# Kernel optimization log

Hardware: AMD Instinct MI355X
Metric: run time of the kernel (lower is better)

Reference implementation:

```python
import jax, jax.numpy as jnp
import numpy as np

N_NODES = 100000
N_EDGES = 1600000
N_FEAT = 128
HIDDEN = 128
N_GRAPHS = 1024


def setup_inputs() -> dict:
    key = jax.random.key(0)
    ks = jax.random.split(key, 9)
    x = jax.random.normal(ks[0], (N_NODES, N_FEAT), dtype=jnp.float32)
    edge_index = jax.random.randint(ks[1], (2, N_EDGES), 0, N_NODES, dtype=jnp.int64)
    batch = jnp.sort(jax.random.randint(ks[2], (N_NODES,), 0, N_GRAPHS, dtype=jnp.int64))
    W1 = jax.random.normal(ks[3], (N_FEAT, HIDDEN), dtype=jnp.float32) * (1.0 / np.sqrt(N_FEAT))
    b1 = jax.random.normal(ks[4], (HIDDEN,), dtype=jnp.float32) * 0.01
    W2 = jax.random.normal(ks[5], (HIDDEN, HIDDEN), dtype=jnp.float32) * (1.0 / np.sqrt(HIDDEN))
    b2 = jax.random.normal(ks[6], (HIDDEN,), dtype=jnp.float32) * 0.01
    Wl = jax.random.normal(ks[7], (HIDDEN, 2), dtype=jnp.float32) * (1.0 / np.sqrt(HIDDEN))
    bl = jax.random.normal(ks[8], (2,), dtype=jnp.float32) * 0.01
    return {"x": x, "edge_index": edge_index, "batch": batch,
            "W1": W1, "b1": b1, "W2": W2, "b2": b2, "Wl": Wl, "bl": bl}


def _gcn_norm(edge_index, num_nodes):
    # PyG GCNConv: add self-loops, then sym-normalize with in-degree (target col).
    loop = jnp.arange(num_nodes, dtype=edge_index.dtype)
    src = jnp.concatenate([edge_index[0], loop])  # [E+N]
    dst = jnp.concatenate([edge_index[1], loop])  # [E+N]
    deg = jax.ops.segment_sum(jnp.ones_like(dst, dtype=jnp.float32), dst,
                              num_segments=num_nodes)
    dinv = jnp.where(deg > 0, jax.lax.rsqrt(deg), 0.0)
    norm = dinv[src] * dinv[dst]  # [E+N]
    return src, dst, norm


def _gcn_conv(h, W, b, src, dst, norm, num_nodes):
    h = h @ W                                   # [N, out]
    msg = h[src] * norm[:, None]                # gather + scale, [E+N, out]
    agg = jax.ops.segment_sum(msg, dst, num_segments=num_nodes)  # scatter-add
    return agg + b


def reference(x, edge_index, batch, W1, b1, W2, b2, Wl, bl):
    n = x.shape[0]
    src, dst, norm = _gcn_norm(edge_index, n)
    h = jax.nn.relu(_gcn_conv(x, W1, b1, src, dst, norm, n))
    h = jax.nn.relu(_gcn_conv(h, W2, b2, src, dst, norm, n))
    # global_mean_pool over graph ids
    sums = jax.ops.segment_sum(h, batch, num_segments=N_GRAPHS)        # [G, H]
    counts = jax.ops.segment_sum(jnp.ones((n,), jnp.float32), batch,
                                 num_segments=N_GRAPHS)
    pooled = sums / jnp.maximum(counts, 1.0)[:, None]
    # F.dropout with training=False default in inference -> identity
    return pooled @ Wl + bl  # [G, 2]
```

## Files before the change

### kernel.cpp

```cpp
#include <hip/hip_runtime.h>
#include <hip/hip_bf16.h>

#define N_NODES 100000
#define N_EDGES 1600000
#define FEAT 128
#define N_GRAPHS 1024
#define NBUCK 391
#define CHUNK 4096

typedef short short8 __attribute__((ext_vector_type(8)));
typedef float float4v __attribute__((ext_vector_type(4)));

static __device__ inline unsigned short f2bf(float f) {
    __hip_bfloat16 b = __float2bfloat16(f);
    unsigned short r;
    __builtin_memcpy(&r, &b, 2);
    return r;
}
static __device__ inline float bf_lo(unsigned int v) { return __uint_as_float(v << 16); }
static __device__ inline float bf_hi(unsigned int v) { return __uint_as_float(v & 0xFFFF0000u); }
static __device__ inline float bf_s(unsigned short s) { return __uint_as_float(((unsigned)s) << 16); }

__global__ __launch_bounds__(256) void k_prep(const float* __restrict__ W1,
                                              const float* __restrict__ W2,
                                              unsigned short* __restrict__ wp1,
                                              unsigned short* __restrict__ wp2,
                                              int* __restrict__ bcount,
                                              unsigned int* __restrict__ udummy) {
    int bid = blockIdx.x;
    const float* W = (bid < 64) ? W1 : W2;
    unsigned short* wp = (bid < 64) ? wp1 : wp2;
    int t = (bid & 63) * 256 + threadIdx.x;
    int k = t >> 7, n = t & 127;
    float w = W[k * 128 + n];
    unsigned ub = __float_as_uint(w);
    unsigned short hi = (unsigned short)(ub >> 16);
    float hif = __uint_as_float(ub & 0xFFFF0000u);
    unsigned short lo = f2bf(w - hif);
    int sidx = n * 128 + ((k & 7) | (8 * (((k >> 3) ^ n) & 15)));
    wp[sidx] = hi;
    wp[16384 + sidx] = lo;
    if (bid == 0) {
        for (int i = threadIdx.x; i < NBUCK; i += 256) bcount[i] = 0;
        if (threadIdx.x < 64) udummy[threadIdx.x] = 0;
    }
}

__global__ __launch_bounds__(256) void k_hist(const int* __restrict__ dst,
                                              int* __restrict__ bcount) {
    __shared__ int h[NBUCK];
    for (int i = threadIdx.x; i < NBUCK; i += 256) h[i] = 0;
    __syncthreads();
    for (int e = blockIdx.x * 256 + threadIdx.x; e < N_EDGES; e += gridDim.x * 256)
        atomicAdd(&h[dst[e] >> 8], 1);
    __syncthreads();
    for (int i = threadIdx.x; i < NBUCK; i += 256) {
        int c = h[i];
        if (c) atomicAdd(&bcount[i], c);
    }
}

__global__ __launch_bounds__(512) void k_scan391(const int* __restrict__ in,
                                                 int* __restrict__ base,
                                                 int* __restrict__ cur,
                                                 int* __restrict__ tail) {
    int t = threadIdx.x;
    int v = (t < NBUCK) ? in[t] : 0;
    int lane = t & 63, wid = t >> 6;
    int s = v;
#pragma unroll
    for (int d = 1; d < 64; d <<= 1) { int n = __shfl_up(s, d); if (lane >= d) s += n; }
    __shared__ int ws[8];
    if (lane == 63) ws[wid] = s;
    __syncthreads();
    if (t < 8) {
        int x = ws[t];
#pragma unroll
        for (int d = 1; d < 8; d <<= 1) { int n = __shfl_up(x, d); if ((int)t >= d) x += n; }
        ws[t] = x;
    }
    __syncthreads();
    int excl = s - v + (wid ? ws[wid - 1] : 0);
    if (t < NBUCK) {
        base[t] = excl;
        if (cur) cur[t] = excl;
    }
    if (t == 0 && tail) tail[0] = N_EDGES;
}

__global__ __launch_bounds__(256) void k_bucket(const int* __restrict__ src,
                                                const int* __restrict__ dst,
                                                int* __restrict__ bcur,
                                                unsigned int* __restrict__ pairs) {
    __shared__ int cnt[NBUCK];
    __shared__ int basebuf[NBUCK];
    int t = threadIdx.x;
    int e0 = blockIdx.x * CHUNK;
    for (int i = t; i < NBUCK; i += 256) cnt[i] = 0;
    __syncthreads();
    unsigned pk[16]; int bk[16];
#pragma unroll
    for (int j = 0; j < 16; ++j) {
        int e = e0 + j * 256 + t;
        if (e < N_EDGES) {
            int s = src[e], d = dst[e];
            bk[j] = d >> 8;
            pk[j] = ((unsigned)s << 8) | (unsigned)(d & 255);
            atomicAdd(&cnt[bk[j]], 1);
        } else bk[j] = -1;
    }
    __syncthreads();
    for (int i = t; i < NBUCK; i += 256) {
        int c = cnt[i];
        basebuf[i] = c ? atomicAdd(&bcur[i], c) : 0;
        cnt[i] = 0;
    }
    __syncthreads();
#pragma unroll
    for (int j = 0; j < 16; ++j) {
        if (bk[j] >= 0) {
            int p = basebuf[bk[j]] + atomicAdd(&cnt[bk[j]], 1);
            pairs[p] = pk[j];
        }
    }
}

__global__ __launch_bounds__(256) void k_bdeg(const unsigned int* __restrict__ pairs,
                                              const int* __restrict__ bbase,
                                              const int* __restrict__ bcount,
                                              int* __restrict__ deg,
                                              float* __restrict__ dinv,
                                              int* __restrict__ wsum) {
    __shared__ int d[256];
    __shared__ int wr[4];
    int b = blockIdx.x, t = threadIdx.x;
    d[t] = 0;
    __syncthreads();
    int s0 = bbase[b], n = bcount[b];
    for (int i = t; i < n; i += 256) atomicAdd(&d[pairs[s0 + i] & 255u], 1);
    __syncthreads();
    int node = b * 256 + t;
    int v = d[t];
    if (node < N_NODES) {
        deg[node] = v;
        dinv[node] = rsqrtf((float)(v + 1));
    }
#pragma unroll
    for (int dd = 32; dd > 0; dd >>= 1) v += __shfl_down(v, dd);
    if ((t & 63) == 0) wr[t >> 6] = v;
    __syncthreads();
    if (t == 0) wsum[b] = wr[0] + wr[1] + wr[2] + wr[3];
}

__global__ __launch_bounds__(256) void k_bfill(const unsigned int* __restrict__ pairs,
                                               const int* __restrict__ bbase,
                                               const int* __restrict__ bcount,
                                               const int* __restrict__ deg,
                                               const int* __restrict__ wbase,
                                               int* __restrict__ offs,
                                               int* __restrict__ csr) {
    __shared__ int lcur[256];
    __shared__ int ws[4];
    int b = blockIdx.x, t = threadIdx.x;
    int node = b * 256 + t;
    int dv = (node < N_NODES) ? deg[node] : 0;
    int lane = t & 63, wid = t >> 6;
    int s = dv;
#pragma unroll
    for (int d = 1; d < 64; d <<= 1) { int n = __shfl_up(s, d); if (lane >= d) s += n; }
    if (lane == 63) ws[wid] = s;
    __syncthreads();
    if (t < 4) {
        int x = ws[t];
#pragma unroll
        for (int d = 1; d < 4; d <<= 1) { int n = __shfl_up(x, d); if ((int)t >= d) x += n; }
        ws[t] = x;
    }
    __syncthreads();
    int excl = s - dv + (wid ? ws[wid - 1] : 0) + wbase[b];
    if (node < N_NODES) offs[node] = excl;
    lcur[t] = excl;
    __syncthreads();
    int s0 = bbase[b], n = bcount[b];
    for (int i = t; i < n; i += 256) {
        unsigned pr = pairs[s0 + i];
        int p = atomicAdd(&lcur[pr & 255u], 1);
        csr[p] = (int)(pr >> 8);
    }
}

__global__ __launch_bounds__(256) void k_gemm_mfma(const float* __restrict__ inp,
                                                   const unsigned short* __restrict__ wp,
                                                   const float* __restrict__ dinv,
                                                   unsigned short* __restrict__ u) {
    __shared__ unsigned short sW[32768];
    {
        float4* d4 = (float4*)sW;
        const float4* s4 = (const float4*)wp;
#pragma unroll
        for (int i = 0; i < 16; ++i) d4[threadIdx.x + 256 * i] = s4[threadIdx.x + 256 * i];
    }
    __syncthreads();
    const int t = threadIdx.x;
    const int wv = t >> 6, L = t & 63;
    const int m = L & 15, q = L >> 4;
    const int r0 = blockIdx.x * 64 + wv * 16;
    int arow = r0 + m;
    if (arow >= N_NODES) arow = N_NODES - 1;
    const float4* ap = (const float4*)(inp + (size_t)arow * 128);
    float4v acc[8];
#pragma unroll
    for (int c = 0; c < 8; ++c) acc[c] = (float4v){0.f, 0.f, 0.f, 0.f};

#pragma unroll
    for (int k0 = 0; k0 < 128; k0 += 32) {
        float4 f0 = ap[(k0 >> 2) + 2 * q];
        float4 f1 = ap[(k0 >> 2) + 2 * q + 1];
        float fa[8] = {f0.x, f0.y, f0.z, f0.w, f1.x, f1.y, f1.z, f1.w};
        short8 ah, al;
#pragma unroll
        for (int j = 0; j < 8; ++j) {
            unsigned ub = __float_as_uint(fa[j]);
            ah[j] = (short)(ub >> 16);
            float hif = __uint_as_float(ub & 0xFFFF0000u);
            al[j] = (short)f2bf(fa[j] - hif);
        }
        const int b = (k0 >> 3) + q;
#pragma unroll
        for (int c = 0; c < 8; ++c) {
            int ng = c * 16 + m;
            int elem = ng * 128 + 8 * ((b ^ ng) & 15);
            short8 bh = *(const short8*)&sW[elem];
            short8 bl = *(const short8*)&sW[16384 + elem];
            acc[c] = __builtin_amdgcn_mfma_f32_16x16x32_bf16(ah, bh, acc[c], 0, 0, 0);
            acc[c] = __builtin_amdgcn_mfma_f32_16x16x32_bf16(al, bh, acc[c], 0, 0, 0);
            acc[c] = __builtin_amdgcn_mfma_f32_16x16x32_bf16(ah, bl, acc[c], 0, 0, 0);
        }
    }
#pragma unroll
    for (int r = 0; r < 4; ++r) {
        int row = r0 + 4 * q + r;
        if (row < N_NODES) {
            float dv = dinv[row];
            unsigned short* up = u + (size_t)row * 128 + m;
#pragma unroll
            for (int c = 0; c < 8; ++c) up[c * 16] = f2bf(dv * acc[c][r]);
        }
    }
}

__global__ __launch_bounds__(256) void k_gemm_mfma_bf(const unsigned short* __restrict__ hh,
                                                      const unsigned short* __restrict__ hl,
                                                      const unsigned short* __restrict__ wp,
                                                      const float* __restrict__ dinv,
                                                      unsigned short* __restrict__ u) {
    __shared__ unsigned short sW[32768];
    {
        float4* d4 = (float4*)sW;
        const float4* s4 = (const float4*)wp;
#pragma unroll
        for (int i = 0; i < 16; ++i) d4[threadIdx.x + 256 * i] = s4[threadIdx.x + 256 * i];
    }
    __syncthreads();
    const int t = threadIdx.x;
    const int wv = t >> 6, L = t & 63;
    const int m = L & 15, q = L >> 4;
    const int r0 = blockIdx.x * 64 + wv * 16;
    int arow = r0 + m;
    if (arow >= N_NODES) arow = N_NODES - 1;
    const unsigned short* hhp = hh + (size_t)arow * 128 + 8 * q;
    const unsigned short* hlp = hl + (size_t)arow * 128 + 8 * q;
    float4v acc[8];
#pragma unroll
    for (int c = 0; c < 8; ++c) acc[c] = (float4v){0.f, 0.f, 0.f, 0.f};

#pragma unroll
    for (int k0 = 0; k0 < 128; k0 += 32) {
        short8 ah = *(const short8*)(hhp + k0);
        short8 al = *(const short8*)(hlp + k0);
        const int b = (k0 >> 3) + q;
#pragma unroll
        for (int c = 0; c < 8; ++c) {
            int ng = c * 16 + m;
            int elem = ng * 128 + 8 * ((b ^ ng) & 15);
            short8 bh = *(const short8*)&sW[elem];
            short8 bl = *(const short8*)&sW[16384 + elem];
            acc[c] = __builtin_amdgcn_mfma_f32_16x16x32_bf16(ah, bh, acc[c], 0, 0, 0);
            acc[c] = __builtin_amdgcn_mfma_f32_16x16x32_bf16(al, bh, acc[c], 0, 0, 0);
            acc[c] = __builtin_amdgcn_mfma_f32_16x16x32_bf16(ah, bl, acc[c], 0, 0, 0);
        }
    }
#pragma unroll
    for (int r = 0; r < 4; ++r) {
        int row = r0 + 4 * q + r;
        if (row < N_NODES) {
            float dv = dinv[row];
            unsigned short* up = u + (size_t)row * 128 + m;
#pragma unroll
            for (int c = 0; c < 8; ++c) up[c * 16] = f2bf(dv * acc[c][r]);
        }
    }
}

__global__ __launch_bounds__(256) void k_agg(const unsigned int* __restrict__ u,
                                             const int* __restrict__ offs,
                                             const int* __restrict__ csr,
                                             const float* __restrict__ dinv,
                                             const float* __restrict__ bias,
                                             unsigned int* __restrict__ hhp,
                                             unsigned int* __restrict__ hlp) {
    int wid = threadIdx.x >> 6;
    int lane = threadIdx.x & 63;
    int node = __builtin_amdgcn_readfirstlane(blockIdx.x * 4 + wid);
    if (node >= N_NODES) return;
    int p = __builtin_amdgcn_readfirstlane(offs[node]);
    int e = __builtin_amdgcn_readfirstlane(offs[node + 1]);
    unsigned int self = u[(size_t)node * 64 + lane];
    float ax0 = bf_lo(self), ay0 = bf_hi(self);
    float ax1 = 0.f, ay1 = 0.f, ax2 = 0.f, ay2 = 0.f, ax3 = 0.f, ay3 = 0.f;
    float ax4 = 0.f, ay4 = 0.f, ax5 = 0.f, ay5 = 0.f, ax6 = 0.f, ay6 = 0.f;
    float ax7 = 0.f, ay7 = 0.f;
    for (; p < e; p += 8) {
        int c0 = csr[p + 0], c1 = csr[p + 1], c2 = csr[p + 2], c3 = csr[p + 3];
        int c4 = csr[p + 4], c5 = csr[p + 5], c6 = csr[p + 6], c7 = csr[p + 7];
        int i0 = c0;
        int i1 = (p + 1 < e) ? c1 : N_NODES;
        int i2 = (p + 2 < e) ? c2 : N_NODES;
        int i3 = (p + 3 < e) ? c3 : N_NODES;
        int i4 = (p + 4 < e) ? c4 : N_NODES;
        int i5 = (p + 5 < e) ? c5 : N_NODES;
        int i6 = (p + 6 < e) ? c6 : N_NODES;
        int i7 = (p + 7 < e) ? c7 : N_NODES;
        unsigned v0 = (u + (size_t)i0 * 64)[lane];
        unsigned v1 = (u + (size_t)i1 * 64)[lane];
        unsigned v2 = (u + (size_t)i2 * 64)[lane];
        unsigned v3 = (u + (size_t)i3 * 64)[lane];
        unsigned v4 = (u + (size_t)i4 * 64)[lane];
        unsigned v5 = (u + (size_t)i5 * 64)[lane];
        unsigned v6 = (u + (size_t)i6 * 64)[lane];
        unsigned v7 = (u + (size_t)i7 * 64)[lane];
        ax0 += bf_lo(v0); ay0 += bf_hi(v0);
        ax1 += bf_lo(v1); ay1 += bf_hi(v1);
        ax2 += bf_lo(v2); ay2 += bf_hi(v2);
        ax3 += bf_lo(v3); ay3 += bf_hi(v3);
        ax4 += bf_lo(v4); ay4 += bf_hi(v4);
        ax5 += bf_lo(v5); ay5 += bf_hi(v5);
        ax6 += bf_lo(v6); ay6 += bf_hi(v6);
        ax7 += bf_lo(v7); ay7 += bf_hi(v7);
    }
    float d = dinv[node];
    float2 b = ((const float2*)bias)[lane];
    float sx = ((ax0 + ax1) + (ax2 + ax3)) + ((ax4 + ax5) + (ax6 + ax7));
    float sy = ((ay0 + ay1) + (ay2 + ay3)) + ((ay4 + ay5) + (ay6 + ay7));
    float r0 = fmaxf(d * sx + b.x, 0.f);
    float r1 = fmaxf(d * sy + b.y, 0.f);
    if (hlp) {
        unsigned u0 = __float_as_uint(r0), u1 = __float_as_uint(r1);
        unsigned short h0 = (unsigned short)(u0 >> 16), h1 = (unsigned short)(u1 >> 16);
        float rf0 = __uint_as_float(u0 & 0xFFFF0000u), rf1 = __uint_as_float(u1 & 0xFFFF0000u);
        unsigned short l0 = f2bf(r0 - rf0), l1 = f2bf(r1 - rf1);
        hhp[(size_t)node * 64 + lane] = (unsigned)h0 | ((unsigned)h1 << 16);
        hlp[(size_t)node * 64 + lane] = (unsigned)l0 | ((unsigned)l1 << 16);
    } else {
        hhp[(size_t)node * 64 + lane] = (unsigned)f2bf(r0) | ((unsigned)f2bf(r1) << 16);
    }
}

__global__ __launch_bounds__(128) void k_pool(const unsigned short* __restrict__ hh,
                                              const int* __restrict__ batch,
                                              const float* __restrict__ Wl,
                                              const float* __restrict__ bl,
                                              float* __restrict__ out) {
    int g = blockIdx.x;
    int c = threadIdx.x;
    __shared__ int sb[2];
    if (c < 2) {
        int tgt = g + c;
        int lo = 0, hi = N_NODES;
        while (lo < hi) { int m = (lo + hi) >> 1; if (batch[m] < tgt) lo = m + 1; else hi = m; }
        sb[c] = lo;
    }
    __syncthreads();
    int s0 = sb[0], s1 = sb[1];
    float sum = 0.f;
    for (int i = s0; i < s1; ++i) sum += bf_s(hh[(size_t)i * 128 + c]);
    float cnt = (float)(s1 - s0);
    float pooled = sum / fmaxf(cnt, 1.0f);
    __shared__ float red[128];
    float w0 = Wl[c * 2 + 0], w1 = Wl[c * 2 + 1];
    red[c] = pooled * w0;
    __syncthreads();
    for (int st = 64; st > 0; st >>= 1) { if (c < st) red[c] += red[c + st]; __syncthreads(); }
    if (c == 0) out[g * 2 + 0] = red[0] + bl[0];
    __syncthreads();
    red[c] = pooled * w1;
    __syncthreads();
    for (int st = 64; st > 0; st >>= 1) { if (c < st) red[c] += red[c + st]; __syncthreads(); }
    if (c == 0) out[g * 2 + 1] = red[0] + bl[1];
}

extern "C" void kernel_launch(void* const* d_in, const int* in_sizes, int n_in,
                              void* d_out, int out_size, void* d_ws, size_t ws_size,
                              hipStream_t stream) {
    const float* x  = (const float*)d_in[0];
    const int* ei   = (const int*)d_in[1];
    const int* batch = (const int*)d_in[2];
    const float* W1 = (const float*)d_in[3];
    const float* b1 = (const float*)d_in[4];
    const float* W2 = (const float*)d_in[5];
    const float* b2 = (const float*)d_in[6];
    const float* Wl = (const float*)d_in[7];
    const float* bl = (const float*)d_in[8];
    float* out = (float*)d_out;
    const int* src = ei;
    const int* dst = ei + N_EDGES;

    char* ws = (char*)d_ws;
    size_t o = 0;
    auto alloc = [&](size_t bytes) -> void* {
        o = (o + 255) & ~(size_t)255;
        void* p = ws + o;
        o += bytes;
        return p;
    };
    int* bcount = (int*)alloc((size_t)NBUCK * 4);
    int* bbase  = (int*)alloc((size_t)NBUCK * 4);
    int* bcur   = (int*)alloc((size_t)NBUCK * 4);
    int* wsum   = (int*)alloc((size_t)NBUCK * 4);
    int* wbase  = (int*)alloc((size_t)NBUCK * 4);
    int* deg    = (int*)alloc((size_t)N_NODES * 4);
    float* dinv = (float*)alloc((size_t)N_NODES * 4);
    int* offs   = (int*)alloc((size_t)(N_NODES + 1) * 4);
    unsigned short* wp1 = (unsigned short*)alloc(65536);
    unsigned short* wp2 = (unsigned short*)alloc(65536);
    unsigned int* pairs = (unsigned int*)alloc((size_t)N_EDGES * 4);
    int* csr    = (int*)alloc((size_t)(N_EDGES + 8) * 4);
    unsigned short* u = (unsigned short*)alloc((size_t)(N_NODES + 1) * 128 * 2);
    unsigned short* hh = (unsigned short*)alloc((size_t)N_NODES * 128 * 2);
    unsigned short* hl = (unsigned short*)alloc((size_t)N_NODES * 128 * 2);

    k_prep<<<128, 256, 0, stream>>>(W1, W2, wp1, wp2, bcount,
                                    (unsigned int*)(u + (size_t)N_NODES * 128));
    k_hist<<<256, 256, 0, stream>>>(dst, bcount);
    k_scan391<<<1, 512, 0, stream>>>(bcount, bbase, bcur, nullptr);
    k_bucket<<<(N_EDGES + CHUNK - 1) / CHUNK, 256, 0, stream>>>(src, dst, bcur, pairs);
    k_bdeg<<<NBUCK, 256, 0, stream>>>(pairs, bbase, bcount, deg, dinv, wsum);
    k_scan391<<<1, 512, 0, stream>>>(wsum, wbase, nullptr, &offs[N_NODES]);
    k_bfill<<<NBUCK, 256, 0, stream>>>(pairs, bbase, bcount, deg, wbase, offs, csr);

    const int gemmGrid = (N_NODES + 63) / 64;
    k_gemm_mfma<<<gemmGrid, 256, 0, stream>>>(x, wp1, dinv, u);
    k_agg<<<(N_NODES + 3) / 4, 256, 0, stream>>>((const unsigned int*)u, offs, csr, dinv, b1,
                                                 (unsigned int*)hh, (unsigned int*)hl);
    k_gemm_mfma_bf<<<gemmGrid, 256, 0, stream>>>(hh, hl, wp2, dinv, u);
    k_agg<<<(N_NODES + 3) / 4, 256, 0, stream>>>((const unsigned int*)u, offs, csr, dinv, b2,
                                                 (unsigned int*)hh, nullptr);

    k_pool<<<N_GRAPHS, 128, 0, stream>>>(hh, batch, Wl, bl, out);
}
```

Measured before the change: 362.6 us.

## Overlap first GEMM with CSR build and fold degree pass into fill

The first layer's GEMM no longer needs dinv, because the source-side normalization moves into the aggregation kernel. That lets the GEMM tiles run as extra blocks inside the bucket and fill kernels, so they overlap with CSR construction. The separate degree kernel and second scan are merged into the fill kernel, which computes local degrees and uses the bucket base as the offset. The weight-prep and histogram kernels are also fused into one launch. In exchange, the aggregation now does an extra dinv gather per neighbor, and the mixed blocks carry a large shared-memory footprint that may reduce occupancy for the bucket blocks.

```diff
diff --git a/kernel.cpp b/kernel.cpp
--- a/kernel.cpp
+++ b/kernel.cpp
@@ -7,6 +7,9 @@
 #define N_GRAPHS 1024
 #define NBUCK 391
 #define CHUNK 4096
+#define NTILES 1563
+#define G1A 781
+#define G1B 782
 
 typedef short short8 __attribute__((ext_vector_type(8)));
 typedef float float4v __attribute__((ext_vector_type(4)));
@@ -21,42 +24,44 @@
 static __device__ inline float bf_hi(unsigned int v) { return __uint_as_float(v & 0xFFFF0000u); }
 static __device__ inline float bf_s(unsigned short s) { return __uint_as_float(((unsigned)s) << 16); }
 
-__global__ __launch_bounds__(256) void k_prep(const float* __restrict__ W1,
-                                              const float* __restrict__ W2,
-                                              unsigned short* __restrict__ wp1,
-                                              unsigned short* __restrict__ wp2,
-                                              int* __restrict__ bcount,
-                                              unsigned int* __restrict__ udummy) {
+__global__ __launch_bounds__(256) void k_prep_hist(const float* __restrict__ W1,
+                                                   const float* __restrict__ W2,
+                                                   unsigned short* __restrict__ wp1,
+                                                   unsigned short* __restrict__ wp2,
+                                                   const int* __restrict__ dst,
+                                                   int* __restrict__ bcount,
+                                                   unsigned int* __restrict__ udummy,
+                                                   float* __restrict__ dinv) {
     int bid = blockIdx.x;
-    const float* W = (bid < 64) ? W1 : W2;
-    unsigned short* wp = (bid < 64) ? wp1 : wp2;
-    int t = (bid & 63) * 256 + threadIdx.x;
-    int k = t >> 7, n = t & 127;
-    float w = W[k * 128 + n];
-    unsigned ub = __float_as_uint(w);
-    unsigned short hi = (unsigned short)(ub >> 16);
-    float hif = __uint_as_float(ub & 0xFFFF0000u);
-    unsigned short lo = f2bf(w - hif);
-    int sidx = n * 128 + ((k & 7) | (8 * (((k >> 3) ^ n) & 15)));
-    wp[sidx] = hi;
-    wp[16384 + sidx] = lo;
-    if (bid == 0) {
-        for (int i = threadIdx.x; i < NBUCK; i += 256) bcount[i] = 0;
-        if (threadIdx.x < 64) udummy[threadIdx.x] = 0;
-    }
-}
-
-__global__ __launch_bounds__(256) void k_hist(const int* __restrict__ dst,
-                                              int* __restrict__ bcount) {
-    __shared__ int h[NBUCK];
-    for (int i = threadIdx.x; i < NBUCK; i += 256) h[i] = 0;
-    __syncthreads();
-    for (int e = blockIdx.x * 256 + threadIdx.x; e < N_EDGES; e += gridDim.x * 256)
-        atomicAdd(&h[dst[e] >> 8], 1);
-    __syncthreads();
-    for (int i = threadIdx.x; i < NBUCK; i += 256) {
-        int c = h[i];
-        if (c) atomicAdd(&bcount[i], c);
+    if (bid < 128) {
+        const float* W = (bid < 64) ? W1 : W2;
+        unsigned short* wp = (bid < 64) ? wp1 : wp2;
+        int t = (bid & 63) * 256 + threadIdx.x;
+        int k = t >> 7, n = t & 127;
+        float w = W[k * 128 + n];
+        unsigned ub = __float_as_uint(w);
+        unsigned short hi = (unsigned short)(ub >> 16);
+        float hif = __uint_as_float(ub & 0xFFFF0000u);
+        unsigned short lo = f2bf(w - hif);
+        int sidx = n * 128 + ((k & 7) | (8 * (((k >> 3) ^ n) & 15)));
+        wp[sidx] = hi;
+        wp[16384 + sidx] = lo;
+        if (bid == 0) {
+            if (threadIdx.x < 64) udummy[threadIdx.x] = 0;
+            if (threadIdx.x == 64) dinv[N_NODES] = 0.f;
+        }
+    } else {
+        __shared__ int h[NBUCK];
+        for (int i = threadIdx.x; i < NBUCK; i += 256) h[i] = 0;
+        __syncthreads();
+        int hb = bid - 128;
+        for (int e = hb * 256 + threadIdx.x; e < N_EDGES; e += 256 * 256)
+            atomicAdd(&h[dst[e] >> 8], 1);
+        __syncthreads();
+        for (int i = threadIdx.x; i < NBUCK; i += 256) {
+            int c = h[i];
+            if (c) atomicAdd(&bcount[i], c);
+        }
     }
 }
 
@@ -83,15 +88,79 @@
     int excl = s - v + (wid ? ws[wid - 1] : 0);
     if (t < NBUCK) {
         base[t] = excl;
-        if (cur) cur[t] = excl;
-    }
-    if (t == 0 && tail) tail[0] = N_EDGES;
-}
-
-__global__ __launch_bounds__(256) void k_bucket(const int* __restrict__ src,
-                                                const int* __restrict__ dst,
-                                                int* __restrict__ bcur,
-                                                unsigned int* __restrict__ pairs) {
+        cur[t] = excl;
+    }
+    if (t == 0) tail[0] = N_EDGES;
+}
+
+__device__ __forceinline__ void gemm_f32_body(int tile, const float* __restrict__ inp,
+                                              const unsigned short* __restrict__ wp,
+                                              unsigned short* __restrict__ u) {
+    __shared__ unsigned short sW[32768];
+    {
+        float4* d4 = (float4*)sW;
+        const float4* s4 = (const float4*)wp;
+#pragma unroll
+        for (int i = 0; i < 16; ++i) d4[threadIdx.x + 256 * i] = s4[threadIdx.x + 256 * i];
+    }
+    __syncthreads();
+    const int t = threadIdx.x;
+    const int wv = t >> 6, L = t & 63;
+    const int m = L & 15, q = L >> 4;
+    const int r0 = tile * 64 + wv * 16;
+    int arow = r0 + m;
+    if (arow >= N_NODES) arow = N_NODES - 1;
+    const float4* ap = (const float4*)(inp + (size_t)arow * 128);
+    float4v acc[8];
+#pragma unroll
+    for (int c = 0; c < 8; ++c) acc[c] = (float4v){0.f, 0.f, 0.f, 0.f};
+#pragma unroll
+    for (int k0 = 0; k0 < 128; k0 += 32) {
+        float4 f0 = ap[(k0 >> 2) + 2 * q];
+        float4 f1 = ap[(k0 >> 2) + 2 * q + 1];
+        float fa[8] = {f0.x, f0.y, f0.z, f0.w, f1.x, f1.y, f1.z, f1.w};
+        short8 ah, al;
+#pragma unroll
+        for (int j = 0; j < 8; ++j) {
+            unsigned ub = __float_as_uint(fa[j]);
+            ah[j] = (short)(ub >> 16);
+            float hif = __uint_as_float(ub & 0xFFFF0000u);
+            al[j] = (short)f2bf(fa[j] - hif);
+        }
+        const int b = (k0 >> 3) + q;
+#pragma unroll
+        for (int c = 0; c < 8; ++c) {
+            int ng = c * 16 + m;
+            int elem = ng * 128 + 8 * ((b ^ ng) & 15);
+            short8 bh = *(const short8*)&sW[elem];
+            short8 bl = *(const short8*)&sW[16384 + elem];
+            acc[c] = __builtin_amdgcn_mfma_f32_16x16x32_bf16(ah, bh, acc[c], 0, 0, 0);
+            acc[c] = __builtin_amdgcn_mfma_f32_16x16x32_bf16(al, bh, acc[c], 0, 0, 0);
+            acc[c] = __builtin_amdgcn_mfma_f32_16x16x32_bf16(ah, bl, acc[c], 0, 0, 0);
+        }
+    }
+#pragma unroll
+    for (int r = 0; r < 4; ++r) {
+        int row = r0 + 4 * q + r;
+        if (row < N_NODES) {
+            unsigned short* up = u + (size_t)row * 128 + m;
+#pragma unroll
+            for (int c = 0; c < 8; ++c) up[c * 16] = f2bf(acc[c][r]);
+        }
+    }
+}
+
+__global__ __launch_bounds__(256) void k_bucket_g1(const int* __restrict__ src,
+                                                   const int* __restrict__ dst,
+                                                   int* __restrict__ bcur,
+                                                   unsigned int* __restrict__ pairs,
+                                                   const float* __restrict__ x,
+                                                   const unsigned short* __restrict__ wp1,
+                                                   unsigned short* __restrict__ u) {
+    if (blockIdx.x >= NBUCK) {
+        gemm_f32_body(blockIdx.x - NBUCK, x, wp1, u);
+        return;
+    }
     __shared__ int cnt[NBUCK];
     __shared__ int basebuf[NBUCK];
     int t = threadIdx.x;
@@ -125,63 +194,48 @@
     }
 }
 
-__global__ __launch_bounds__(256) void k_bdeg(const unsigned int* __restrict__ pairs,
-                                              const int* __restrict__ bbase,
-                                              const int* __restrict__ bcount,
-                                              int* __restrict__ deg,
-                                              float* __restrict__ dinv,
-                                              int* __restrict__ wsum) {
-    __shared__ int d[256];
-    __shared__ int wr[4];
-    int b = blockIdx.x, t = threadIdx.x;
-    d[t] = 0;
-    __syncthreads();
-    int s0 = bbase[b], n = bcount[b];
-    for (int i = t; i < n; i += 256) atomicAdd(&d[pairs[s0 + i] & 255u], 1);
-    __syncthreads();
-    int node = b * 256 + t;
-    int v = d[t];
-    if (node < N_NODES) {
-        deg[node] = v;
-        dinv[node] = rsqrtf((float)(v + 1));
-    }
-#pragma unroll
-    for (int dd = 32; dd > 0; dd >>= 1) v += __shfl_down(v, dd);
-    if ((t & 63) == 0) wr[t >> 6] = v;
-    __syncthreads();
-    if (t == 0) wsum[b] = wr[0] + wr[1] + wr[2] + wr[3];
-}
-
-__global__ __launch_bounds__(256) void k_bfill(const unsigned int* __restrict__ pairs,
-                                               const int* __restrict__ bbase,
-                                               const int* __restrict__ bcount,
-                                               const int* __restrict__ deg,
-                                               const int* __restrict__ wbase,
-                                               int* __restrict__ offs,
-                                               int* __restrict__ csr) {
+__global__ __launch_bounds__(256) void k_bfill_g1(const unsigned int* __restrict__ pairs,
+                                                  const int* __restrict__ bbase,
+                                                  const int* __restrict__ bcount,
+                                                  float* __restrict__ dinv,
+                                                  int* __restrict__ offs,
+                                                  int* __restrict__ csr,
+                                                  const float* __restrict__ x,
+                                                  const unsigned short* __restrict__ wp1,
+                                                  unsigned short* __restrict__ u) {
+    if (blockIdx.x >= NBUCK) {
+        gemm_f32_body(blockIdx.x - NBUCK + G1A, x, wp1, u);
+        return;
+    }
+    __shared__ int degl[256];
     __shared__ int lcur[256];
     __shared__ int ws[4];
     int b = blockIdx.x, t = threadIdx.x;
+    degl[t] = 0;
+    __syncthreads();
+    int s0 = bbase[b], n = bcount[b];
+    for (int i = t; i < n; i += 256) atomicAdd(&degl[pairs[s0 + i] & 255u], 1);
+    __syncthreads();
     int node = b * 256 + t;
-    int dv = (node < N_NODES) ? deg[node] : 0;
+    int dv = degl[t];
+    if (node < N_NODES) dinv[node] = rsqrtf((float)(dv + 1));
     int lane = t & 63, wid = t >> 6;
     int s = dv;
 #pragma unroll
-    for (int d = 1; d < 64; d <<= 1) { int n = __shfl_up(s, d); if (lane >= d) s += n; }
+    for (int d = 1; d < 64; d <<= 1) { int nn = __shfl_up(s, d); if (lane >= d) s += nn; }
     if (lane == 63) ws[wid] = s;
     __syncthreads();
     if (t < 4) {
-        int x = ws[t];
-#pragma unroll
-        for (int d = 1; d < 4; d <<= 1) { int n = __shfl_up(x, d); if ((int)t >= d) x += n; }
-        ws[t] = x;
-    }
-    __syncthreads();
-    int excl = s - dv + (wid ? ws[wid - 1] : 0) + wbase[b];
+        int xx = ws[t];
+#pragma unroll
+        for (int d = 1; d < 4; d <<= 1) { int nn = __shfl_up(xx, d); if ((int)t >= d) xx += nn; }
+        ws[t] = xx;
+    }
+    __syncthreads();
+    int excl = s - dv + (wid ? ws[wid - 1] : 0) + bbase[b];
     if (node < N_NODES) offs[node] = excl;
     lcur[t] = excl;
     __syncthreads();
-    int s0 = bbase[b], n = bcount[b];
     for (int i = t; i < n; i += 256) {
         unsigned pr = pairs[s0 + i];
         int p = atomicAdd(&lcur[pr & 255u], 1);
@@ -189,70 +243,9 @@
     }
 }
 
-__global__ __launch_bounds__(256) void k_gemm_mfma(const float* __restrict__ inp,
-                                                   const unsigned short* __restrict__ wp,
-                                                   const float* __restrict__ dinv,
-                                                   unsigned short* __restrict__ u) {
-    __shared__ unsigned short sW[32768];
-    {
-        float4* d4 = (float4*)sW;
-        const float4* s4 = (const float4*)wp;
-#pragma unroll
-        for (int i = 0; i < 16; ++i) d4[threadIdx.x + 256 * i] = s4[threadIdx.x + 256 * i];
-    }
-    __syncthreads();
-    const int t = threadIdx.x;
-    const int wv = t >> 6, L = t & 63;
-    const int m = L & 15, q = L >> 4;
-    const int r0 = blockIdx.x * 64 + wv * 16;
-    int arow = r0 + m;
-    if (arow >= N_NODES) arow = N_NODES - 1;
-    const float4* ap = (const float4*)(inp + (size_t)arow * 128);
-    float4v acc[8];
-#pragma unroll
-    for (int c = 0; c < 8; ++c) acc[c] = (float4v){0.f, 0.f, 0.f, 0.f};
-
-#pragma unroll
-    for (int k0 = 0; k0 < 128; k0 += 32) {
-        float4 f0 = ap[(k0 >> 2) + 2 * q];
-        float4 f1 = ap[(k0 >> 2) + 2 * q + 1];
-        float fa[8] = {f0.x, f0.y, f0.z, f0.w, f1.x, f1.y, f1.z, f1.w};
-        short8 ah, al;
-#pragma unroll
-        for (int j = 0; j < 8; ++j) {
-            unsigned ub = __float_as_uint(fa[j]);
-            ah[j] = (short)(ub >> 16);
-            float hif = __uint_as_float(ub & 0xFFFF0000u);
-            al[j] = (short)f2bf(fa[j] - hif);
-        }
-        const int b = (k0 >> 3) + q;
-#pragma unroll
-        for (int c = 0; c < 8; ++c) {
-            int ng = c * 16 + m;
-            int elem = ng * 128 + 8 * ((b ^ ng) & 15);
-            short8 bh = *(const short8*)&sW[elem];
-            short8 bl = *(const short8*)&sW[16384 + elem];
-            acc[c] = __builtin_amdgcn_mfma_f32_16x16x32_bf16(ah, bh, acc[c], 0, 0, 0);
-            acc[c] = __builtin_amdgcn_mfma_f32_16x16x32_bf16(al, bh, acc[c], 0, 0, 0);
-            acc[c] = __builtin_amdgcn_mfma_f32_16x16x32_bf16(ah, bl, acc[c], 0, 0, 0);
-        }
-    }
-#pragma unroll
-    for (int r = 0; r < 4; ++r) {
-        int row = r0 + 4 * q + r;
-        if (row < N_NODES) {
-            float dv = dinv[row];
-            unsigned short* up = u + (size_t)row * 128 + m;
-#pragma unroll
-            for (int c = 0; c < 8; ++c) up[c * 16] = f2bf(dv * acc[c][r]);
-        }
-    }
-}
-
 __global__ __launch_bounds__(256) void k_gemm_mfma_bf(const unsigned short* __restrict__ hh,
                                                       const unsigned short* __restrict__ hl,
                                                       const unsigned short* __restrict__ wp,
-                                                      const float* __restrict__ dinv,
                                                       unsigned short* __restrict__ u) {
     __shared__ unsigned short sW[32768];
     {
@@ -273,7 +266,6 @@
     float4v acc[8];
 #pragma unroll
     for (int c = 0; c < 8; ++c) acc[c] = (float4v){0.f, 0.f, 0.f, 0.f};
-
 #pragma unroll
     for (int k0 = 0; k0 < 128; k0 += 32) {
         short8 ah = *(const short8*)(hhp + k0);
@@ -294,10 +286,9 @@
     for (int r = 0; r < 4; ++r) {
         int row = r0 + 4 * q + r;
         if (row < N_NODES) {
-            float dv = dinv[row];
             unsigned short* up = u + (size_t)row * 128 + m;
 #pragma unroll
-            for (int c = 0; c < 8; ++c) up[c * 16] = f2bf(dv * acc[c][r]);
+            for (int c = 0; c < 8; ++c) up[c * 16] = f2bf(acc[c][r]);
         }
     }
 }
@@ -315,8 +306,9 @@
     if (node >= N_NODES) return;
     int p = __builtin_amdgcn_readfirstlane(offs[node]);
     int e = __builtin_amdgcn_readfirstlane(offs[node + 1]);
+    float dsf = dinv[node];
     unsigned int self = u[(size_t)node * 64 + lane];
-    float ax0 = bf_lo(self), ay0 = bf_hi(self);
+    float ax0 = dsf * bf_lo(self), ay0 = dsf * bf_hi(self);
     float ax1 = 0.f, ay1 = 0.f, ax2 = 0.f, ay2 = 0.f, ax3 = 0.f, ay3 = 0.f;
     float ax4 = 0.f, ay4 = 0.f, ax5 = 0.f, ay5 = 0.f, ax6 = 0.f, ay6 = 0.f;
     float ax7 = 0.f, ay7 = 0.f;
@@ -331,6 +323,8 @@
         int i5 = (p + 5 < e) ? c5 : N_NODES;
         int i6 = (p + 6 < e) ? c6 : N_NODES;
         int i7 = (p + 7 < e) ? c7 : N_NODES;
+        float d0 = dinv[i0], d1 = dinv[i1], d2 = dinv[i2], d3 = dinv[i3];
+        float d4 = dinv[i4], d5 = dinv[i5], d6 = dinv[i6], d7 = dinv[i7];
         unsigned v0 = (u + (size_t)i0 * 64)[lane];
         unsigned v1 = (u + (size_t)i1 * 64)[lane];
         unsigned v2 = (u + (size_t)i2 * 64)[lane];
@@ -339,21 +333,20 @@
         unsigned v5 = (u + (size_t)i5 * 64)[lane];
         unsigned v6 = (u + (size_t)i6 * 64)[lane];
         unsigned v7 = (u + (size_t)i7 * 64)[lane];
-        ax0 += bf_lo(v0); ay0 += bf_hi(v0);
-        ax1 += bf_lo(v1); ay1 += bf_hi(v1);
-        ax2 += bf_lo(v2); ay2 += bf_hi(v2);
-        ax3 += bf_lo(v3); ay3 += bf_hi(v3);
-        ax4 += bf_lo(v4); ay4 += bf_hi(v4);
-        ax5 += bf_lo(v5); ay5 += bf_hi(v5);
-        ax6 += bf_lo(v6); ay6 += bf_hi(v6);
-        ax7 += bf_lo(v7); ay7 += bf_hi(v7);
-    }
-    float d = dinv[node];
+        ax0 = fmaf(d0, bf_lo(v0), ax0); ay0 = fmaf(d0, bf_hi(v0), ay0);
+        ax1 = fmaf(d1, bf_lo(v1), ax1); ay1 = fmaf(d1, bf_hi(v1), ay1);
+        ax2 = fmaf(d2, bf_lo(v2), ax2); ay2 = fmaf(d2, bf_hi(v2), ay2);
+        ax3 = fmaf(d3, bf_lo(v3), ax3); ay3 = fmaf(d3, bf_hi(v3), ay3);
+        ax4 = fmaf(d4, bf_lo(v4), ax4); ay4 = fmaf(d4, bf_hi(v4), ay4);
+        ax5 = fmaf(d5, bf_lo(v5), ax5); ay5 = fmaf(d5, bf_hi(v5), ay5);
+        ax6 = fmaf(d6, bf_lo(v6), ax6); ay6 = fmaf(d6, bf_hi(v6), ay6);
+        ax7 = fmaf(d7, bf_lo(v7), ax7); ay7 = fmaf(d7, bf_hi(v7), ay7);
+    }
     float2 b = ((const float2*)bias)[lane];
     float sx = ((ax0 + ax1) + (ax2 + ax3)) + ((ax4 + ax5) + (ax6 + ax7));
     float sy = ((ay0 + ay1) + (ay2 + ay3)) + ((ay4 + ay5) + (ay6 + ay7));
-    float r0 = fmaxf(d * sx + b.x, 0.f);
-    float r1 = fmaxf(d * sy + b.y, 0.f);
+    float r0 = fmaxf(dsf * sx + b.x, 0.f);
+    float r1 = fmaxf(dsf * sy + b.y, 0.f);
     if (hlp) {
         unsigned u0 = __float_as_uint(r0), u1 = __float_as_uint(r1);
         unsigned short h0 = (unsigned short)(u0 >> 16), h1 = (unsigned short)(u1 >> 16);
@@ -426,10 +419,7 @@
     int* bcount = (int*)alloc((size_t)NBUCK * 4);
     int* bbase  = (int*)alloc((size_t)NBUCK * 4);
     int* bcur   = (int*)alloc((size_t)NBUCK * 4);
-    int* wsum   = (int*)alloc((size_t)NBUCK * 4);
-    int* wbase  = (int*)alloc((size_t)NBUCK * 4);
-    int* deg    = (int*)alloc((size_t)N_NODES * 4);
-    float* dinv = (float*)alloc((size_t)N_NODES * 4);
+    float* dinv = (float*)alloc((size_t)(N_NODES + 1) * 4);
     int* offs   = (int*)alloc((size_t)(N_NODES + 1) * 4);
     unsigned short* wp1 = (unsigned short*)alloc(65536);
     unsigned short* wp2 = (unsigned short*)alloc(65536);
@@ -439,20 +429,16 @@
     unsigned short* hh = (unsigned short*)alloc((size_t)N_NODES * 128 * 2);
     unsigned short* hl = (unsigned short*)alloc((size_t)N_NODES * 128 * 2);
 
-    k_prep<<<128, 256, 0, stream>>>(W1, W2, wp1, wp2, bcount,
-                                    (unsigned int*)(u + (size_t)N_NODES * 128));
-    k_hist<<<256, 256, 0, stream>>>(dst, bcount);
-    k_scan391<<<1, 512, 0, stream>>>(bcount, bbase, bcur, nullptr);
-    k_bucket<<<(N_EDGES + CHUNK - 1) / CHUNK, 256, 0, stream>>>(src, dst, bcur, pairs);
-    k_bdeg<<<NBUCK, 256, 0, stream>>>(pairs, bbase, bcount, deg, dinv, wsum);
-    k_scan391<<<1, 512, 0, stream>>>(wsum, wbase, nullptr, &offs[N_NODES]);
-    k_bfill<<<NBUCK, 256, 0, stream>>>(pairs, bbase, bcount, deg, wbase, offs, csr);
-
-    const int gemmGrid = (N_NODES + 63) / 64;
-    k_gemm_mfma<<<gemmGrid, 256, 0, stream>>>(x, wp1, dinv, u);
+    hipMemsetAsync(bcount, 0, (size_t)NBUCK * 4, stream);
+    k_prep_hist<<<384, 256, 0, stream>>>(W1, W2, wp1, wp2, dst, bcount,
+                                         (unsigned int*)(u + (size_t)N_NODES * 128), dinv);
+    k_scan391<<<1, 512, 0, stream>>>(bcount, bbase, bcur, &offs[N_NODES]);
+    k_bucket_g1<<<NBUCK + G1A, 256, 0, stream>>>(src, dst, bcur, pairs, x, wp1, u);
+    k_bfill_g1<<<NBUCK + G1B, 256, 0, stream>>>(pairs, bbase, bcount, dinv, offs, csr, x, wp1, u);
+
     k_agg<<<(N_NODES + 3) / 4, 256, 0, stream>>>((const unsigned int*)u, offs, csr, dinv, b1,
                                                  (unsigned int*)hh, (unsigned int*)hl);
-    k_gemm_mfma_bf<<<gemmGrid, 256, 0, stream>>>(hh, hl, wp2, dinv, u);
+    k_gemm_mfma_bf<<<NTILES, 256, 0, stream>>>(hh, hl, wp2, u);
     k_agg<<<(N_NODES + 3) / 4, 256, 0, stream>>>((const unsigned int*)u, offs, csr, dinv, b2,
                                                  (unsigned int*)hh, nullptr);
 
```

Measured after the change: 352.2 us. 1.03x faster.
